# Performance work log

Measured on AMD Instinct MI355X. Metric: run time of the kernel, lower is better.

The kernel has to match this reference:

```python
import jax, jax.numpy as jnp
import numpy as np

B, S, H = 2, 2048, 4096
NH, NKV, HD = 32, 8, 128
THETA = 1000000.0
NEG = jnp.finfo(jnp.float32).min


def setup_inputs() -> dict:
    key = jax.random.key(0)
    ks = jax.random.split(key, 9)
    s = 0.02
    return {
        "hidden_states": jax.random.normal(ks[0], (B, S, H), jnp.float32),
        "position_ids": jnp.tile(jnp.arange(S, dtype=jnp.int32)[None, :], (B, 1)),
        "Wq": jax.random.normal(ks[1], (NH * HD, H), jnp.float32) * s,
        "bq": jax.random.normal(ks[2], (NH * HD,), jnp.float32) * s,
        "Wk": jax.random.normal(ks[3], (NKV * HD, H), jnp.float32) * s,
        "bk": jax.random.normal(ks[4], (NKV * HD,), jnp.float32) * s,
        "Wv": jax.random.normal(ks[5], (NKV * HD, H), jnp.float32) * s,
        "bv": jax.random.normal(ks[6], (NKV * HD,), jnp.float32) * s,
        "Wo": jax.random.normal(ks[7], (H, H), jnp.float32) * s,
        "bo": jax.random.normal(ks[8], (H,), jnp.float32) * s,
    }


def _rotate_half_interleaved(x):
    # y[..., ::2] = -x[..., 1::2]; y[..., 1::2] = x[..., ::2]
    x2 = x.reshape(*x.shape[:-1], -1, 2)
    y = jnp.stack([-x2[..., 1], x2[..., 0]], axis=-1)
    return y.reshape(x.shape)


def reference(hidden_states, position_ids, Wq, bq, Wk, bk, Wv, bv, Wo, bo):
    bsz, q_len, _ = hidden_states.shape
    q = (hidden_states @ Wq.T + bq).reshape(bsz, q_len, NH, HD).transpose(0, 2, 1, 3)
    k = (hidden_states @ Wk.T + bk).reshape(bsz, q_len, NKV, HD).transpose(0, 2, 1, 3)
    v = (hidden_states @ Wv.T + bv).reshape(bsz, q_len, NKV, HD).transpose(0, 2, 1, 3)

    # rotary embedding (interleaved / repeat_interleave variant)
    inv_freq = 1.0 / (THETA ** (jnp.arange(0, HD, 2, dtype=jnp.float32) / HD))
    freqs = position_ids.astype(jnp.float32)[:, :, None] * inv_freq[None, None, :]  # [B,S,HD/2]
    emb = jnp.repeat(freqs, 2, axis=-1)  # [B,S,HD]
    cos = jnp.cos(emb)[:, None, :, :]  # [B,1,S,HD]
    sin = jnp.sin(emb)[:, None, :, :]
    q = q * cos + _rotate_half_interleaved(q) * sin
    k = k * cos + _rotate_half_interleaved(k) * sin

    # GQA: repeat KV heads (repeat_interleave on head axis)
    n_rep = NH // NKV
    k = jnp.repeat(k, n_rep, axis=1)
    v = jnp.repeat(v, n_rep, axis=1)

    scores = jnp.einsum("bhqd,bhkd->bhqk", q, k) / np.sqrt(HD).astype(np.float32)
    causal = jnp.tril(jnp.ones((q_len, q_len), dtype=bool))
    scores = jnp.where(causal[None, None, :, :], scores, NEG)
    attn = jax.nn.softmax(scores.astype(jnp.float32), axis=-1).astype(q.dtype)
    out = jnp.einsum("bhqk,bhkd->bhqd", attn, v)
    out = out.transpose(0, 2, 1, 3).reshape(bsz, q_len, H)
    return out @ Wo.T + bo
```

## Files before the change

### kernel.cpp

```cpp
#include <hip/hip_runtime.h>
#include <stdint.h>

typedef __bf16 bf16x8 __attribute__((ext_vector_type(8)));
typedef float f32x4 __attribute__((ext_vector_type(4)));
typedef float f32x16 __attribute__((ext_vector_type(16)));

#define S_LEN 2048
#define NKVH 8
#define HDIM 128
#define MROWS 4096
#define LDQKV 6144
#define SCALE 0.08838834764831845f
#define C_LOG2 0.1275405707067851f
#define THR_RAW 62.7f
#define ROPE_L2 0.31143075889569023f

__device__ __forceinline__ unsigned short f2bf(float f) {
  unsigned u = __float_as_uint(f);
  u += 0x7FFFu + ((u >> 16) & 1u);
  return (unsigned short)(u >> 16);
}
__device__ __forceinline__ float bf2f(unsigned short h) {
  return __uint_as_float(((unsigned)h) << 16);
}

__device__ __forceinline__ void gload16(const unsigned short* g, unsigned short* l) {
  __builtin_amdgcn_global_load_lds(
      (__attribute__((address_space(1))) void*)(g),
      (__attribute__((address_space(3))) void*)(l), 16, 0, 0);
}

__global__ void cast4(const float4* __restrict__ s0, const float4* __restrict__ s1,
                      const float4* __restrict__ s2, const float4* __restrict__ s3,
                      ushort4* __restrict__ d0, ushort4* __restrict__ d1,
                      ushort4* __restrict__ d2, ushort4* __restrict__ d3) {
  const int b = blockIdx.x;
  const float4* s; ushort4* d; int lb;
  if (b < 1024)      { s = s0; d = d0; lb = b; }
  else if (b < 2048) { s = s1; d = d1; lb = b - 1024; }
  else if (b < 2304) { s = s2; d = d2; lb = b - 2048; }
  else               { s = s3; d = d3; lb = b - 2304; }
  int base = lb * 4096 + threadIdx.x;
#pragma unroll
  for (int i = 0; i < 16; i++) {
    float4 v = s[base + i * 256];
    ushort4 o;
    o.x = f2bf(v.x); o.y = f2bf(v.y); o.z = f2bf(v.z); o.w = f2bf(v.w);
    d[base + i * 256] = o;
  }
}

__global__ void cast_f32_bf16(const float4* __restrict__ in, ushort4* __restrict__ out, int n4) {
  int i = blockIdx.x * 256 + threadIdx.x;
  const int stride = gridDim.x * 256;
  for (; i < n4; i += stride) {
    float4 v = in[i];
    ushort4 o;
    o.x = f2bf(v.x); o.y = f2bf(v.y); o.z = f2bf(v.z); o.w = f2bf(v.w);
    out[i] = o;
  }
}

template <int OUTF, int ROPE>
__global__ __launch_bounds__(512, 2)
void gemm256(const unsigned short* __restrict__ A,
             const unsigned short* __restrict__ Bw,
             const float* __restrict__ bias,
             void* __restrict__ C,
             const int* __restrict__ pos,
             int ldc, int K) {
  __shared__ unsigned short lds[8][8192];

  const int t = threadIdx.x;
  const int lane = t & 63;
  const int w = t >> 6;
  const int wr = w >> 2, wc = w & 3;
  const int row16 = lane & 15, kgrp = lane >> 4;
  const int m0 = blockIdx.y * 256, n0 = blockIdx.x * 256;

  const int riu = t >> 3;
  const int col = (((t & 7) ^ (riu & 7)) << 3);
  const int rB0 = (riu & 31) + ((riu >> 5) << 6);
  const unsigned short* pA = A + (size_t)(m0 + riu) * K + col;
  const unsigned short* pB = Bw + (size_t)(n0 + rB0) * K + col;

#define STGU(SL, SRC)                                                       \
  {                                                                         \
    gload16((SRC), &lds[SL][t * 8]);                                        \
    gload16((SRC) + (size_t)128 * K, &lds[SL][4096 + t * 8]);               \
  }
#define RDA(SL)                                                             \
  _Pragma("unroll") for (int mi = 0; mi < 4; mi++)                          \
  _Pragma("unroll") for (int ks = 0; ks < 2; ks++)                          \
    afr[mi][ks] = *(const bf16x8*)(&lds[SL][0] + abase + mi * 1024 +        \
                                   ((((ks << 2) + kgrp) ^ sw) << 3));
#define RDB(SL, W)                                                          \
  _Pragma("unroll") for (int nj = 0; nj < 2; nj++)                          \
  _Pragma("unroll") for (int ks = 0; ks < 2; ks++)                          \
    bfr[W][nj][ks] = *(const bf16x8*)(&lds[SL][0] + bbase + nj * 1024 +     \
                                      ((((ks << 2) + kgrp) ^ sw) << 3));
#define MM(MO, NO, W)                                                       \
  __builtin_amdgcn_s_setprio(1);                                            \
  _Pragma("unroll") for (int mi = 0; mi < 4; mi++)                          \
  _Pragma("unroll") for (int nj = 0; nj < 2; nj++)                          \
  _Pragma("unroll") for (int ks = 0; ks < 2; ks++)                          \
    acc[(MO) + mi][(NO) + nj] = __builtin_amdgcn_mfma_f32_16x16x32_bf16(    \
        afr[mi][ks], bfr[W][nj][ks], acc[(MO) + mi][(NO) + nj], 0, 0, 0);   \
  __builtin_amdgcn_s_setprio(0);
#define BAR __builtin_amdgcn_s_barrier()

  const int sw = row16 & 7;
  const int abase = (wr * 64 + row16) * 64;
  const int bbase = (wc * 32 + row16) * 64;

  f32x4 acc[8][4];
#pragma unroll
  for (int i = 0; i < 8; i++)
#pragma unroll
    for (int j = 0; j < 4; j++) acc[i][j] = (f32x4){0.f, 0.f, 0.f, 0.f};

  bf16x8 afr[4][2], bfr[2][2][2];
  const int NT = K >> 6;
  const int NI = NT >> 1;

  STGU(0, pA);
  STGU(1, pB);
  STGU(2, pB + (size_t)32 * K);
  STGU(3, pA + (size_t)64 * K);
  STGU(4, pA + 64);
  STGU(5, pB + 64);
  STGU(6, pB + (size_t)32 * K + 64);
  asm volatile("s_waitcnt vmcnt(6)" ::: "memory");
  BAR;

  for (int I = 0; I < NI; ++I) {
    const size_t k1 = ((size_t)(2 * I + 1)) << 6;
    const size_t k2 = ((size_t)(2 * I + 2)) << 6;
    const size_t k3 = ((size_t)(2 * I + 3)) << 6;
    const bool s2 = (I + 1 < NI);

    RDA(0); RDB(1, 0);
    STGU(7, pA + (size_t)64 * K + k1);
    BAR;
    MM(0, 0, 0);
    BAR;
    RDB(2, 1);
    if (s2) STGU(0, pA + k2);
    BAR;
    MM(0, 2, 1);
    BAR;
    RDA(3);
    if (s2) STGU(1, pB + k2);
    BAR;
    MM(4, 2, 1);
    BAR;
    if (s2) {
      STGU(2, pB + (size_t)32 * K + k2);
      asm volatile("s_waitcnt vmcnt(6)" ::: "memory");
    } else {
      asm volatile("s_waitcnt vmcnt(0)" ::: "memory");
    }
    BAR;
    MM(4, 0, 0);
    BAR;
    RDA(4); RDB(5, 0);
    if (s2) STGU(3, pA + (size_t)64 * K + k2);
    BAR;
    MM(0, 0, 0);
    BAR;
    RDB(6, 1);
    if (s2) STGU(4, pA + k3);
    BAR;
    MM(0, 2, 1);
    BAR;
    RDA(7);
    if (s2) STGU(5, pB + k3);
    BAR;
    MM(4, 2, 1);
    BAR;
    if (s2) {
      STGU(6, pB + (size_t)32 * K + k3);
      asm volatile("s_waitcnt vmcnt(6)" ::: "memory");
    } else {
      asm volatile("s_waitcnt vmcnt(0)" ::: "memory");
    }
    BAR;
    MM(4, 0, 0);
    BAR;
  }
#undef STGU
#undef RDA
#undef RDB
#undef MM
#undef BAR

#pragma unroll
  for (int MI = 0; MI < 8; MI++) {
#pragma unroll
    for (int NJ = 0; NJ < 4; NJ++) {
      const int gr = m0 + wr * 128 + MI * 16 + kgrp * 4;
      const int gc = n0 + wc * 64 + NJ * 16 + row16;
      const float bv = bias[gc];
      if (ROPE) {
        const int hf = (gc & 127) >> 1;
        const float inv = exp2f(-(float)hf * ROPE_L2);
#pragma unroll
        for (int jj = 0; jj < 4; jj++) {
          float v = acc[MI][NJ][jj] + bv;
          float px = __shfl_xor(v, 1);
          float sn, cs;
          __sincosf((float)pos[gr + jj] * inv, &sn, &cs);
          float ov = (gc & 1) ? fmaf(v, cs, px * sn) : fmaf(v, cs, -px * sn);
          ((unsigned short*)C)[(size_t)(gr + jj) * ldc + gc] = f2bf(ov);
        }
      } else {
#pragma unroll
        for (int jj = 0; jj < 4; jj++) {
          float v = acc[MI][NJ][jj] + bv;
          if (OUTF) ((float*)C)[(size_t)(gr + jj) * ldc + gc] = v;
          else ((unsigned short*)C)[(size_t)(gr + jj) * ldc + gc] = f2bf(v);
        }
      }
    }
  }
}

template <int OUTF, int ROPE>
__global__ __launch_bounds__(512, 2)
void gemm128(const unsigned short* __restrict__ A,
             const unsigned short* __restrict__ Bw,
             const float* __restrict__ bias,
             void* __restrict__ C,
             const int* __restrict__ pos,
             int ldc, int K) {
  __shared__ unsigned short lds[3 * 24576];

  const int t = threadIdx.x;
  const int lane = t & 63;
  const int w = t >> 6;
  const int wr = w >> 2, wc = w & 3;
  const int row16 = lane & 15, kgrp = lane >> 4;
  const int m0 = blockIdx.y * 128, n0 = blockIdx.x * 256;

  const int riu = t >> 3;
  const int col = (((t & 7) ^ (riu & 7)) << 3);
  const unsigned short* pA = A + (size_t)(m0 + riu) * K + col;
  const unsigned short* pB = Bw + (size_t)(n0 + riu) * K + col;

#define STG6(bo_, kk_)                                                      \
  {                                                                         \
    gload16(pA + (kk_), &lds[(bo_) + t * 8]);                               \
    gload16(pA + (size_t)64 * K + (kk_), &lds[(bo_) + 4096 + t * 8]);       \
    gload16(pB + (kk_), &lds[(bo_) + 8192 + t * 8]);                        \
    gload16(pB + (size_t)64 * K + (kk_), &lds[(bo_) + 12288 + t * 8]);      \
    gload16(pB + (size_t)128 * K + (kk_), &lds[(bo_) + 16384 + t * 8]);     \
    gload16(pB + (size_t)192 * K + (kk_), &lds[(bo_) + 20480 + t * 8]);     \
  }

  const int sw = row16 & 7;
  const int abase = (wr * 64 + row16) * 64;
  const int bbase = 8192 + (wc * 64 + row16) * 64;

  f32x4 acc[4][4];
#pragma unroll
  for (int i = 0; i < 4; i++)
#pragma unroll
    for (int j = 0; j < 4; j++) acc[i][j] = (f32x4){0.f, 0.f, 0.f, 0.f};

  bf16x8 afr[4][2], bfr[4][2];
  const int NT = K >> 6;

  STG6(0, 0);
  STG6(24576, 64);

  int rbc = 0;
  int rbs = 2;
  for (int T = 0; T < NT; ++T) {
    if (T < NT - 1) { asm volatile("s_waitcnt vmcnt(6)\n\ts_barrier" ::: "memory"); }
    else            { asm volatile("s_waitcnt vmcnt(0)\n\ts_barrier" ::: "memory"); }
    if (T + 2 < NT) STG6(rbs * 24576, (size_t)(T + 2) << 6);
    const unsigned short* Lc = &lds[rbc * 24576];

#pragma unroll
    for (int mi = 0; mi < 4; mi++)
#pragma unroll
      for (int ks = 0; ks < 2; ks++)
        afr[mi][ks] = *(const bf16x8*)(Lc + abase + mi * 1024 + ((((ks << 2) + kgrp) ^ sw) << 3));
#pragma unroll
    for (int nj = 0; nj < 4; nj++)
#pragma unroll
      for (int ks = 0; ks < 2; ks++)
        bfr[nj][ks] = *(const bf16x8*)(Lc + bbase + nj * 1024 + ((((ks << 2) + kgrp) ^ sw) << 3));

    __builtin_amdgcn_s_setprio(1);
#pragma unroll
    for (int mi = 0; mi < 4; mi++)
#pragma unroll
      for (int nj = 0; nj < 4; nj++)
#pragma unroll
        for (int ks = 0; ks < 2; ks++)
          acc[mi][nj] = __builtin_amdgcn_mfma_f32_16x16x32_bf16(afr[mi][ks], bfr[nj][ks], acc[mi][nj], 0, 0, 0);
    __builtin_amdgcn_s_setprio(0);

    rbc++; if (rbc == 3) rbc = 0;
    rbs++; if (rbs == 3) rbs = 0;
  }
#undef STG6

#pragma unroll
  for (int MI = 0; MI < 4; MI++) {
#pragma unroll
    for (int NJ = 0; NJ < 4; NJ++) {
      const int gr = m0 + wr * 64 + MI * 16 + kgrp * 4;
      const int gc = n0 + wc * 64 + NJ * 16 + row16;
      const float bv = bias[gc];
      if (ROPE && gc < 1024) {
        const int hf = (gc & 127) >> 1;
        const float inv = exp2f(-(float)hf * ROPE_L2);
#pragma unroll
        for (int jj = 0; jj < 4; jj++) {
          float v = acc[MI][NJ][jj] + bv;
          float px = __shfl_xor(v, 1);
          float sn, cs;
          __sincosf((float)pos[gr + jj] * inv, &sn, &cs);
          float ov = (gc & 1) ? fmaf(v, cs, px * sn) : fmaf(v, cs, -px * sn);
          ((unsigned short*)C)[(size_t)(gr + jj) * ldc + gc] = f2bf(ov);
        }
      } else {
#pragma unroll
        for (int jj = 0; jj < 4; jj++) {
          float v = acc[MI][NJ][jj] + bv;
          if (OUTF) ((float*)C)[(size_t)(gr + jj) * ldc + gc] = v;
          else ((unsigned short*)C)[(size_t)(gr + jj) * ldc + gc] = f2bf(v);
        }
      }
    }
  }
}

__global__ void transpose_v(const unsigned short* __restrict__ V, int ldv,
                            unsigned short* __restrict__ Vt) {
  __shared__ unsigned short tile[32][40];
  const int t = threadIdx.x;
  const int n0 = blockIdx.x * 32;
  const int m0 = blockIdx.y * 32;
  const int r = t >> 3;
  const int c = (t & 7) << 2;
  const unsigned short* src = V + (size_t)(m0 + r) * ldv + n0 + c;
  ushort4 d = *(const ushort4*)src;
  tile[r][c] = d.x; tile[r][c + 1] = d.y; tile[r][c + 2] = d.z; tile[r][c + 3] = d.w;
  __syncthreads();
  const int b = m0 >> 11;
  unsigned short* dst = Vt + (size_t)(b * 1024 + n0 + r) * 2048 + (m0 & 2047) + c;
  ushort4 o;
  o.x = tile[c][r]; o.y = tile[c + 1][r]; o.z = tile[c + 2][r]; o.w = tile[c + 3][r];
  *(ushort4*)dst = o;
}

__global__ __launch_bounds__(256, 2)
void attn_kernel4(const unsigned short* __restrict__ QKV,
                  const unsigned short* __restrict__ Vt,
                  unsigned short* __restrict__ O) {
  __shared__ unsigned short sK[2 * 128 * 64];
  __shared__ unsigned short sV[2 * 128 * 64];

  const int t = threadIdx.x;
  const int lane = t & 63;
  const int w = t >> 6;
  const int l31 = lane & 31;
  const int hi = lane >> 5;
  const int bid = blockIdx.x;
  const int g = bid >> 6, bh = bid & 63;
  const int qt = (g < 8) ? (15 - g) : (g - 8);
  const int b = bh >> 5, h = bh & 31;
  const int kh = h >> 2;
  const int q0 = qt << 7;
  const int qw = q0 + w * 32;
  const int qg = qw + l31;

  const int ntiles = qt + 1;
  const int myTiles = (qw + 159) >> 7;

  const int r5 = t >> 3;
  const int psw = ((t & 7) ^ (r5 & 7)) << 3;
  const unsigned short* Kp = QKV + (size_t)(b * S_LEN) * LDQKV + 4096 + kh * HDIM;
  const unsigned short* Vp = Vt + (size_t)(b * 1024 + kh * HDIM) * 2048;
  const unsigned short* KpA = Kp + (size_t)r5 * LDQKV + psw;
  const unsigned short* VpA = Vp + (size_t)r5 * 2048 + psw;

#define STAGE(kv0m)                                                            \
  {                                                                            \
    _Pragma("unroll")                                                          \
    for (int p = 0; p < 8; p++)                                                \
      gload16(KpA + (size_t)((kv0m) + ((p & 3) << 5)) * LDQKV + ((p >> 2) << 6), \
              &sK[p * 2048 + t * 8]);                                          \
    _Pragma("unroll")                                                          \
    for (int p = 0; p < 8; p++)                                                \
      gload16(VpA + (size_t)((p & 3) << 5) * 2048 + (kv0m) + ((p >> 2) << 6),  \
              &sV[p * 2048 + t * 8]);                                          \
  }

  bf16x8 qf[8];
  {
    const unsigned short* qb = QKV + (size_t)(b * S_LEN + qw + l31) * LDQKV + h * HDIM + hi * 8;
#pragma unroll
    for (int kd = 0; kd < 8; kd++) qf[kd] = *(const bf16x8*)(qb + kd * 16);
  }

  f32x16 o[4];
#pragma unroll
  for (int nt = 0; nt < 4; nt++)
#pragma unroll
    for (int r = 0; r < 16; r++) o[nt][r] = 0.f;
  float m = -1e30f, lsum = 0.f;

  const int rw7 = (l31 & 7) << 4;
  const int kswz = (hi << 4) ^ rw7;
  const int rbase = l31 << 6;

  for (int it = 0; it < ntiles; ++it) {
    STAGE(it << 7);
    asm volatile("s_waitcnt vmcnt(0)" ::: "memory");
    __builtin_amdgcn_s_barrier();

    if (it < myTiles) {
      const int kv0 = it << 7;

      f32x16 st[4];
#pragma unroll
      for (int r = 0; r < 16; r++) { st[0][r] = 0.f; st[1][r] = 0.f; st[2][r] = 0.f; st[3][r] = 0.f; }
      __builtin_amdgcn_s_setprio(1);
#pragma unroll
      for (int kd = 0; kd < 8; kd++) {
        const int koff = ((kd >> 2) << 13) + ((((kd & 3) << 5) ^ kswz) >> 1);
        bf16x8 k0 = *(const bf16x8*)(sK + koff + rbase);
        bf16x8 k1 = *(const bf16x8*)(sK + koff + rbase + 2048);
        bf16x8 k2 = *(const bf16x8*)(sK + koff + rbase + 4096);
        bf16x8 k3 = *(const bf16x8*)(sK + koff + rbase + 6144);
        st[0] = __builtin_amdgcn_mfma_f32_32x32x16_bf16(k0, qf[kd], st[0], 0, 0, 0);
        st[1] = __builtin_amdgcn_mfma_f32_32x32x16_bf16(k1, qf[kd], st[1], 0, 0, 0);
        st[2] = __builtin_amdgcn_mfma_f32_32x32x16_bf16(k2, qf[kd], st[2], 0, 0, 0);
        st[3] = __builtin_amdgcn_mfma_f32_32x32x16_bf16(k3, qf[kd], st[3], 0, 0, 0);
      }
      __builtin_amdgcn_s_setprio(0);

      if (it == myTiles - 1) {
#pragma unroll
        for (int s2 = 0; s2 < 4; s2++)
#pragma unroll
          for (int r = 0; r < 16; r++) {
            const int kvg = kv0 + s2 * 32 + (r & 3) + 8 * (r >> 2) + 4 * hi;
            if (kvg > qg) st[s2][r] = -1e30f;
          }
      }

      float mx[8];
#pragma unroll
      for (int r = 0; r < 8; r++)
        mx[r] = fmaxf(fmaxf(fmaxf(st[0][r], st[0][r + 8]), fmaxf(st[1][r], st[1][r + 8])),
                      fmaxf(fmaxf(st[2][r], st[2][r + 8]), fmaxf(st[3][r], st[3][r + 8])));
#pragma unroll
      for (int d = 4; d >= 1; d >>= 1)
#pragma unroll
        for (int r = 0; r < d; r++) mx[r] = fmaxf(mx[r], mx[r + d]);
      float tmax = fmaxf(mx[0], __shfl_xor(mx[0], 32));

      if (!__all(tmax <= m + THR_RAW)) {
        const float mnew = fmaxf(m, tmax);
        const float corr = exp2f((m - mnew) * C_LOG2);
        lsum *= corr;
#pragma unroll
        for (int r = 0; r < 16; r++) {
          const int src = (r & 3) + 8 * (r >> 2) + 4 * hi;
          const float cr = __shfl(corr, src);
#pragma unroll
          for (int nt = 0; nt < 4; nt++) o[nt][r] *= cr;
        }
        m = mnew;
      }
      const float mC = m * C_LOG2;

#pragma unroll
      for (int s2 = 0; s2 < 4; s2++)
#pragma unroll
        for (int r = 0; r < 16; r++) st[s2][r] = exp2f(fmaf(st[s2][r], C_LOG2, -mC));
      float sm[8];
#pragma unroll
      for (int r = 0; r < 8; r++)
        sm[r] = ((st[0][r] + st[0][r + 8]) + (st[1][r] + st[1][r + 8])) +
                ((st[2][r] + st[2][r + 8]) + (st[3][r] + st[3][r + 8]));
#pragma unroll
      for (int d = 4; d >= 1; d >>= 1)
#pragma unroll
        for (int r = 0; r < d; r++) sm[r] += sm[r + d];
      float tsum = sm[0] + __shfl_xor(sm[0], 32);
      lsum += tsum;

      bf16x8 pa[8];
#pragma unroll
      for (int s2 = 0; s2 < 4; s2++) {
        unsigned pw[8];
#pragma unroll
        for (int i = 0; i < 8; i++)
          asm("v_cvt_pk_bf16_f32 %0, %1, %2" : "=v"(pw[i]) : "v"(st[s2][2 * i]), "v"(st[s2][2 * i + 1]));
        const unsigned y0 = hi ? pw[0] : pw[2];
        const unsigned y1 = hi ? pw[1] : pw[3];
        const unsigned y2 = hi ? pw[4] : pw[6];
        const unsigned y3 = hi ? pw[5] : pw[7];
        const unsigned x0 = (unsigned)__shfl_xor((int)y0, 32);
        const unsigned x1 = (unsigned)__shfl_xor((int)y1, 32);
        const unsigned x2 = (unsigned)__shfl_xor((int)y2, 32);
        const unsigned x3 = (unsigned)__shfl_xor((int)y3, 32);
        union { unsigned u[4]; bf16x8 v; } u0, u1;
        u0.u[0] = hi ? x0 : pw[0];
        u0.u[1] = hi ? x1 : pw[1];
        u0.u[2] = hi ? pw[2] : x0;
        u0.u[3] = hi ? pw[3] : x1;
        u1.u[0] = hi ? x2 : pw[4];
        u1.u[1] = hi ? x3 : pw[5];
        u1.u[2] = hi ? pw[6] : x2;
        u1.u[3] = hi ? pw[7] : x3;
        pa[2 * s2] = u0.v; pa[2 * s2 + 1] = u1.v;
      }

      __builtin_amdgcn_s_setprio(1);
#pragma unroll
      for (int nt = 0; nt < 4; nt++) {
        const unsigned short* vr = sV + nt * 2048 + rbase;
#pragma unroll
        for (int ks = 0; ks < 8; ks++) {
          bf16x8 vb = *(const bf16x8*)(vr + ((ks >> 2) << 13) + ((((ks & 3) << 5) ^ kswz) >> 1));
          o[nt] = __builtin_amdgcn_mfma_f32_32x32x16_bf16(pa[ks], vb, o[nt], 0, 0, 0);
        }
      }
      __builtin_amdgcn_s_setprio(0);
    }

    __builtin_amdgcn_s_barrier();
  }

  const float linv = 1.0f / lsum;
#pragma unroll
  for (int r = 0; r < 16; r++) {
    const int qr = (r & 3) + 8 * (r >> 2) + 4 * hi;
    const float lr = __shfl(linv, qr);
    unsigned short* orow = O + (size_t)(b * S_LEN + qw + qr) * 4096 + h * HDIM + l31;
#pragma unroll
    for (int nt = 0; nt < 4; nt++) orow[nt * 32] = f2bf(o[nt][r] * lr);
  }
#undef STAGE
}

extern "C" void kernel_launch(void* const* d_in, const int* in_sizes, int n_in,
                              void* d_out, int out_size, void* d_ws, size_t ws_size,
                              hipStream_t stream) {
  const float* hs = (const float*)d_in[0];
  const int*  pos = (const int*)d_in[1];
  const float* Wq = (const float*)d_in[2];
  const float* bq = (const float*)d_in[3];
  const float* Wk = (const float*)d_in[4];
  const float* bk = (const float*)d_in[5];
  const float* Wv = (const float*)d_in[6];
  const float* bv = (const float*)d_in[7];
  const float* Wo = (const float*)d_in[8];
  const float* bo = (const float*)d_in[9];
  float* out = (float*)d_out;

  char* ws = (char*)d_ws;
  unsigned short* hbf  = (unsigned short*)(ws);
  unsigned short* Wbuf = (unsigned short*)(ws + 33554432);
  unsigned short* QKV  = (unsigned short*)(ws + 83886080);
  unsigned short* Vtb  = (unsigned short*)(ws + 134217728);
  float*          biasb= (float*)(ws + 142606336);

  cast4<<<2560, 256, 0, stream>>>(
      (const float4*)hs, (const float4*)Wq, (const float4*)Wk, (const float4*)Wv,
      (ushort4*)hbf, (ushort4*)Wbuf, (ushort4*)(Wbuf + 16777216), (ushort4*)(Wbuf + 20971520));
  hipMemcpyAsync(biasb, bq, 4096 * 4, hipMemcpyDeviceToDevice, stream);
  hipMemcpyAsync(biasb + 4096, bk, 1024 * 4, hipMemcpyDeviceToDevice, stream);
  hipMemcpyAsync(biasb + 5120, bv, 1024 * 4, hipMemcpyDeviceToDevice, stream);

  gemm256<0, 1><<<dim3(16, 16), 512, 0, stream>>>(hbf, Wbuf, biasb, QKV, pos, LDQKV, 4096);
  gemm128<0, 1><<<dim3(8, 32), 512, 0, stream>>>(hbf, Wbuf + 16777216, biasb + 4096, QKV + 4096, pos, LDQKV, 4096);

  cast_f32_bf16<<<2048, 256, 0, stream>>>((const float4*)Wo, (ushort4*)Wbuf, 4194304);

  transpose_v<<<dim3(32, 128), 256, 0, stream>>>(QKV + 5120, LDQKV, Vtb);

  attn_kernel4<<<dim3(1024), 256, 0, stream>>>(QKV, Vtb, hbf);

  gemm256<1, 0><<<dim3(16, 16), 512, 0, stream>>>(hbf, Wbuf, bo, out, nullptr, 4096, 4096);
}
```

Baseline: 506.0 us.

## Swizzle GEMM block order across XCDs and split attention K/V load waits

GEMM kernels now launch as 1D grids and remap the block index so that consecutive blocks on the same XCD (bid&7) cover neighbouring tiles, with the aim of improving L2 reuse of A/B tiles. In attention, K and V staging are issued separately. The kernel waits only for the K loads (vmcnt(8)) before computing QK^T and softmax, then waits for V before the PV MFMAs, so V loads overlap the score computation. The cost is an extra barrier per tile, plus the pa fragment array being hoisted outside the conditional.

```diff
diff --git a/kernel.cpp b/kernel.cpp
--- a/kernel.cpp
+++ b/kernel.cpp
@@ -76,7 +76,9 @@
   const int w = t >> 6;
   const int wr = w >> 2, wc = w & 3;
   const int row16 = lane & 15, kgrp = lane >> 4;
-  const int m0 = blockIdx.y * 256, n0 = blockIdx.x * 256;
+  const int bid = blockIdx.x;
+  const int swz = (bid & 7) * 32 + (bid >> 3);
+  const int m0 = (swz >> 4) * 256, n0 = (swz & 15) * 256;
 
   const int riu = t >> 3;
   const int col = (((t & 7) ^ (riu & 7)) << 3);
@@ -240,7 +242,9 @@
   const int w = t >> 6;
   const int wr = w >> 2, wc = w & 3;
   const int row16 = lane & 15, kgrp = lane >> 4;
-  const int m0 = blockIdx.y * 128, n0 = blockIdx.x * 256;
+  const int bid = blockIdx.x;
+  const int swz = (bid & 7) * 32 + (bid >> 3);
+  const int m0 = (swz >> 3) * 128, n0 = (swz & 7) * 256;
 
   const int riu = t >> 3;
   const int col = (((t & 7) ^ (riu & 7)) << 3);
@@ -388,12 +392,15 @@
   const unsigned short* KpA = Kp + (size_t)r5 * LDQKV + psw;
   const unsigned short* VpA = Vp + (size_t)r5 * 2048 + psw;
 
-#define STAGE(kv0m)                                                            \
+#define STAGE_K(kv0m)                                                          \
   {                                                                            \
     _Pragma("unroll")                                                          \
     for (int p = 0; p < 8; p++)                                                \
       gload16(KpA + (size_t)((kv0m) + ((p & 3) << 5)) * LDQKV + ((p >> 2) << 6), \
               &sK[p * 2048 + t * 8]);                                          \
+  }
+#define STAGE_V(kv0m)                                                          \
+  {                                                                            \
     _Pragma("unroll")                                                          \
     for (int p = 0; p < 8; p++)                                                \
       gload16(VpA + (size_t)((p & 3) << 5) * 2048 + (kv0m) + ((p >> 2) << 6),  \
@@ -419,11 +426,15 @@
   const int rbase = l31 << 6;
 
   for (int it = 0; it < ntiles; ++it) {
-    STAGE(it << 7);
-    asm volatile("s_waitcnt vmcnt(0)" ::: "memory");
+    STAGE_K(it << 7);
+    STAGE_V(it << 7);
+    asm volatile("s_waitcnt vmcnt(8)" ::: "memory");
     __builtin_amdgcn_s_barrier();
 
-    if (it < myTiles) {
+    const bool act = (it < myTiles);
+    bf16x8 pa[8];
+
+    if (act) {
       const int kv0 = it << 7;
 
       f32x16 st[4];
@@ -496,7 +507,6 @@
       float tsum = sm[0] + __shfl_xor(sm[0], 32);
       lsum += tsum;
 
-      bf16x8 pa[8];
 #pragma unroll
       for (int s2 = 0; s2 < 4; s2++) {
         unsigned pw[8];
@@ -522,7 +532,12 @@
         u1.u[3] = hi ? pw[7] : x3;
         pa[2 * s2] = u0.v; pa[2 * s2 + 1] = u1.v;
       }
-
+    }
+
+    asm volatile("s_waitcnt vmcnt(0)" ::: "memory");
+    __builtin_amdgcn_s_barrier();
+
+    if (act) {
       __builtin_amdgcn_s_setprio(1);
 #pragma unroll
       for (int nt = 0; nt < 4; nt++) {
@@ -548,7 +563,8 @@
 #pragma unroll
     for (int nt = 0; nt < 4; nt++) orow[nt * 32] = f2bf(o[nt][r] * lr);
   }
-#undef STAGE
+#undef STAGE_K
+#undef STAGE_V
 }
 
 extern "C" void kernel_launch(void* const* d_in, const int* in_sizes, int n_in,
@@ -580,8 +596,8 @@
   hipMemcpyAsync(biasb + 4096, bk, 1024 * 4, hipMemcpyDeviceToDevice, stream);
   hipMemcpyAsync(biasb + 5120, bv, 1024 * 4, hipMemcpyDeviceToDevice, stream);
 
-  gemm256<0, 1><<<dim3(16, 16), 512, 0, stream>>>(hbf, Wbuf, biasb, QKV, pos, LDQKV, 4096);
-  gemm128<0, 1><<<dim3(8, 32), 512, 0, stream>>>(hbf, Wbuf + 16777216, biasb + 4096, QKV + 4096, pos, LDQKV, 4096);
+  gemm256<0, 1><<<dim3(256), 512, 0, stream>>>(hbf, Wbuf, biasb, QKV, pos, LDQKV, 4096);
+  gemm128<0, 1><<<dim3(256), 512, 0, stream>>>(hbf, Wbuf + 16777216, biasb + 4096, QKV + 4096, pos, LDQKV, 4096);
 
   cast_f32_bf16<<<2048, 256, 0, stream>>>((const float4*)Wo, (ushort4*)Wbuf, 4194304);
 
@@ -589,5 +605,5 @@
 
   attn_kernel4<<<dim3(1024), 256, 0, stream>>>(QKV, Vtb, hbf);
 
-  gemm256<1, 0><<<dim3(16, 16), 512, 0, stream>>>(hbf, Wbuf, bo, out, nullptr, 4096, 4096);
-}
+  gemm256<1, 0><<<dim3(256), 512, 0, stream>>>(hbf, Wbuf, bo, out, nullptr, 4096, 4096);
+}
```

Measured after the change: 499.2 us. No clear change (-1.3%).
